# Optimization experiments

Hardware: AMD Instinct MI355X
Metric: run time of the kernel (lower is better)

## Reference

```python
import jax, jax.numpy as jnp
import numpy as np

N = 100_000        # nodes
F_IN = 1024        # input features
H1, C1 = 8, 8      # layer-1 heads, per-head channels (concat -> 64)
C_OUT = 40         # num classes (layer-2, heads=1, concat=False)
E = 3_200_000      # directed edges (avg degree 32)
NEG_SLOPE = 0.2    # PyG GATConv default leaky_relu slope


def setup_inputs() -> dict:
    key = jax.random.key(0)
    ks = jax.random.split(key, 10)
    x = jax.random.normal(ks[0], (N, F_IN), jnp.float32)
    edge_index = jax.random.randint(ks[1], (2, E), 0, N, dtype=jnp.int32)
    s1 = 1.0 / np.sqrt(F_IN)
    W1 = jax.random.normal(ks[2], (F_IN, H1 * C1), jnp.float32) * s1
    sa = 1.0 / np.sqrt(C1)
    att_src1 = jax.random.normal(ks[3], (H1, C1), jnp.float32) * sa
    att_dst1 = jax.random.normal(ks[4], (H1, C1), jnp.float32) * sa
    b1 = jnp.zeros((H1 * C1,), jnp.float32)
    s2 = 1.0 / np.sqrt(H1 * C1)
    W2 = jax.random.normal(ks[5], (H1 * C1, C_OUT), jnp.float32) * s2
    so = 1.0 / np.sqrt(C_OUT)
    att_src2 = jax.random.normal(ks[6], (1, C_OUT), jnp.float32) * so
    att_dst2 = jax.random.normal(ks[7], (1, C_OUT), jnp.float32) * so
    b2 = jnp.zeros((C_OUT,), jnp.float32)
    return {"x": x, "edge_index": edge_index, "W1": W1, "att_src1": att_src1,
            "att_dst1": att_dst1, "b1": b1, "W2": W2, "att_src2": att_src2,
            "att_dst2": att_dst2, "b2": b2}


def gat_layer(x, src, dst, W, a_src, a_dst, b, heads, ch, concat, n):
    # per-head linear projection: [n, heads, ch]
    xw = (x @ W).reshape(n, heads, ch)
    # per-node attention logits: [n, heads]
    al_src = jnp.einsum('nhc,hc->nh', xw, a_src)
    al_dst = jnp.einsum('nhc,hc->nh', xw, a_dst)
    # per-edge scores (message src -> dst): [e, heads]
    e = jax.nn.leaky_relu(al_src[src] + al_dst[dst], NEG_SLOPE)
    # segment softmax over incoming edges of each dst node
    m = jax.ops.segment_max(e, dst, num_segments=n)          # [n, heads]
    p = jnp.exp(e - m[dst])
    denom = jax.ops.segment_sum(p, dst, num_segments=n)      # [n, heads]
    alpha = p / (denom[dst] + 1e-16)                          # [e, heads]
    # weighted scatter-sum of source features
    out = jax.ops.segment_sum(xw[src] * alpha[:, :, None], dst, num_segments=n)
    out = out.reshape(n, heads * ch) if concat else out.mean(axis=1)
    return out + b


def reference(x, edge_index, W1, att_src1, att_dst1, b1, W2, att_src2, att_dst2, b2):
    n = x.shape[0]
    # PyG GATConv default: add self loops
    loop = jnp.arange(n, dtype=edge_index.dtype)
    src = jnp.concatenate([edge_index[0], loop])
    dst = jnp.concatenate([edge_index[1], loop])
    h = jax.nn.elu(gat_layer(x, src, dst, W1, att_src1, att_dst1, b1, H1, C1, True, n))
    h = gat_layer(h, src, dst, W2, att_src2, att_dst2, b2, 1, C_OUT, False, n)
    return jax.nn.log_softmax(h, axis=1)
```

## Files before the change

kernel.cpp:

```cpp
#include <hip/hip_runtime.h>
#include <hip/hip_bf16.h>
#include <cstdint>
#include <cstddef>

#define F_IN 1024
#define F1 64
#define H1 8
#define C1 8
#define C_OUT 40
#define XW2S 64
#define NEG 0.2f
#define LOG2E 1.442695040888963387f
#define B1 256
#define BSHIFT 9
#define BNODES 512

typedef __attribute__((ext_vector_type(8))) short short8;
typedef __attribute__((ext_vector_type(4))) float f32x4;

static __device__ __forceinline__ unsigned short f2bf(float f) {
  union { float f; unsigned u; } v; v.f = f;
  unsigned r = v.u + 0x7fff + ((v.u >> 16) & 1);
  return (unsigned short)(r >> 16);
}
static __device__ __forceinline__ float bf2f(unsigned short h) {
  union { unsigned u; float f; } v; v.u = ((unsigned)h) << 16; return v.f;
}
static __device__ __forceinline__ unsigned pkbf(float a, float b) {
  union { __hip_bfloat162 h; unsigned u; } c;
  c.h = __float22bfloat162_rn(float2{a, b});
  return c.u;
}
static __device__ __forceinline__ int rfl(int v) {
  return __builtin_amdgcn_readfirstlane(v);
}

__global__ __launch_bounds__(256) void w1cvt_kernel(const float* __restrict__ W1,
                                                    unsigned short* __restrict__ w1t) {
  int i = blockIdx.x * 256 + threadIdx.x;
  int c = i >> 10, k = i & 1023;
  w1t[i] = f2bf(W1[(size_t)k * F1 + c]);
}

__global__ __launch_bounds__(256) void gemm1_mfma(const float* __restrict__ x,
                                                  const unsigned short* __restrict__ w1t,
                                                  unsigned short* __restrict__ xw1, int n) {
  const int tid = threadIdx.x;
  const int wv = tid >> 6;
  const int l = tid & 63;
  const int lr = l & 15;
  const int lg = l >> 4;
  const int rowBase = blockIdx.x * 128 + wv * 32;
  int r0 = rowBase + lr, r1 = rowBase + 16 + lr;
  int r0c = r0 < n ? r0 : (n - 1);
  int r1c = r1 < n ? r1 : (n - 1);
  const float* px0 = x + (size_t)r0c * F_IN + lg * 8;
  const float* px1 = x + (size_t)r1c * F_IN + lg * 8;

  f32x4 acc00 = {0.f,0.f,0.f,0.f}, acc01 = acc00, acc02 = acc00, acc03 = acc00;
  f32x4 acc10 = acc00, acc11 = acc00, acc12 = acc00, acc13 = acc00;

#pragma unroll 2
  for (int k0 = 0; k0 < F_IN; k0 += 32) {
    float4 xa0 = *(const float4*)(px0 + k0);
    float4 xb0 = *(const float4*)(px0 + k0 + 4);
    float4 xa1 = *(const float4*)(px1 + k0);
    float4 xb1 = *(const float4*)(px1 + k0 + 4);
    union { short8 s; unsigned u[4]; } a0, a1;
    a0.u[0] = pkbf(xa0.x, xa0.y); a0.u[1] = pkbf(xa0.z, xa0.w);
    a0.u[2] = pkbf(xb0.x, xb0.y); a0.u[3] = pkbf(xb0.z, xb0.w);
    a1.u[0] = pkbf(xa1.x, xa1.y); a1.u[1] = pkbf(xa1.z, xa1.w);
    a1.u[2] = pkbf(xb1.x, xb1.y); a1.u[3] = pkbf(xb1.z, xb1.w);
    const size_t kOff = (size_t)(k0 + lg * 8);
    short8 b0 = *(const short8*)(w1t + (size_t)(0 * 16 + lr) * F_IN + kOff);
    short8 b1 = *(const short8*)(w1t + (size_t)(1 * 16 + lr) * F_IN + kOff);
    short8 b2 = *(const short8*)(w1t + (size_t)(2 * 16 + lr) * F_IN + kOff);
    short8 b3 = *(const short8*)(w1t + (size_t)(3 * 16 + lr) * F_IN + kOff);
    acc00 = __builtin_amdgcn_mfma_f32_16x16x32_bf16(a0.s, b0, acc00, 0, 0, 0);
    acc01 = __builtin_amdgcn_mfma_f32_16x16x32_bf16(a0.s, b1, acc01, 0, 0, 0);
    acc02 = __builtin_amdgcn_mfma_f32_16x16x32_bf16(a0.s, b2, acc02, 0, 0, 0);
    acc03 = __builtin_amdgcn_mfma_f32_16x16x32_bf16(a0.s, b3, acc03, 0, 0, 0);
    acc10 = __builtin_amdgcn_mfma_f32_16x16x32_bf16(a1.s, b0, acc10, 0, 0, 0);
    acc11 = __builtin_amdgcn_mfma_f32_16x16x32_bf16(a1.s, b1, acc11, 0, 0, 0);
    acc12 = __builtin_amdgcn_mfma_f32_16x16x32_bf16(a1.s, b2, acc12, 0, 0, 0);
    acc13 = __builtin_amdgcn_mfma_f32_16x16x32_bf16(a1.s, b3, acc13, 0, 0, 0);
  }

#pragma unroll
  for (int r = 0; r < 4; ++r) {
    int o0 = rowBase + lg * 4 + r;
    if (o0 < n) {
      unsigned short* po = xw1 + (size_t)o0 * F1 + lr;
      po[0]  = f2bf(acc00[r]);
      po[16] = f2bf(acc01[r]);
      po[32] = f2bf(acc02[r]);
      po[48] = f2bf(acc03[r]);
    }
    int o1 = rowBase + 16 + lg * 4 + r;
    if (o1 < n) {
      unsigned short* po = xw1 + (size_t)o1 * F1 + lr;
      po[0]  = f2bf(acc10[r]);
      po[16] = f2bf(acc11[r]);
      po[32] = f2bf(acc12[r]);
      po[48] = f2bf(acc13[r]);
    }
  }
}

__global__ __launch_bounds__(256) void al1_kernel(const unsigned short* __restrict__ xw1,
    const float* __restrict__ asrc, const float* __restrict__ adst,
    float* __restrict__ al_src, float* __restrict__ al_dst, int n) {
  int id = blockIdx.x * 256 + threadIdx.x;
  if (id >= n * H1) return;
  int node = id >> 3, h = id & 7;
  const unsigned short* row = xw1 + (size_t)node * F1 + h * C1;
  float s = 0.f, d = 0.f;
#pragma unroll
  for (int c = 0; c < C1; ++c) {
    float v = bf2f(row[c]);
    s += v * asrc[h * C1 + c];
    d += v * adst[h * C1 + c];
  }
  al_src[id] = s * LOG2E;
  al_dst[id] = d * LOG2E;
}

__global__ __launch_bounds__(256) void binhist_kernel(const int* __restrict__ dst,
    int* __restrict__ cnt, int e, int nbuck) {
  __shared__ int lh[256];
  int tid = threadIdx.x, blk = blockIdx.x;
  lh[tid] = 0;
  __syncthreads();
  int chunk = (e + gridDim.x - 1) / gridDim.x;
  int s = blk * chunk, en = min(e, s + chunk);
  for (int i = s + tid; i < en; i += 256) atomicAdd(&lh[dst[i] >> BSHIFT], 1);
  __syncthreads();
  if (tid < nbuck) cnt[tid * B1 + blk] = lh[tid];
}

__global__ __launch_bounds__(256) void scan1_kernel(const int* __restrict__ in,
    int* __restrict__ excl, int* __restrict__ bsum, int len) {
  __shared__ int s[256];
  int tid = threadIdx.x;
  int gid = blockIdx.x * 256 + tid;
  int v = gid < len ? in[gid] : 0;
  s[tid] = v;
  __syncthreads();
  for (int ofs = 1; ofs < 256; ofs <<= 1) {
    int t = (tid >= ofs) ? s[tid - ofs] : 0;
    __syncthreads();
    s[tid] += t;
    __syncthreads();
  }
  if (gid < len) excl[gid] = s[tid] - v;
  if (tid == 255) bsum[blockIdx.x] = s[255];
}

__global__ __launch_bounds__(1024) void scan2_kernel(int* __restrict__ bsum, int nb) {
  __shared__ int s[1024];
  int tid = threadIdx.x;
  int v = tid < nb ? bsum[tid] : 0;
  s[tid] = v;
  __syncthreads();
  for (int ofs = 1; ofs < 1024; ofs <<= 1) {
    int t = (tid >= ofs) ? s[tid - ofs] : 0;
    __syncthreads();
    s[tid] += t;
    __syncthreads();
  }
  if (tid < nb) bsum[tid] = s[tid] - v;
}

__global__ __launch_bounds__(256) void binscatter_kernel(const int* __restrict__ src,
    const int* __restrict__ dst, const int* __restrict__ cntS,
    const int* __restrict__ bsum, unsigned* __restrict__ binned, int e, int nbuck) {
  __shared__ int lcur[256];
  int tid = threadIdx.x, blk = blockIdx.x;
  if (tid < nbuck) lcur[tid] = cntS[tid * B1 + blk] + bsum[tid];
  __syncthreads();
  int chunk = (e + gridDim.x - 1) / gridDim.x;
  int s = blk * chunk, en = min(e, s + chunk);
  for (int i = s + tid; i < en; i += 256) {
    int d = dst[i];
    int pos = atomicAdd(&lcur[d >> BSHIFT], 1);
    binned[pos] = ((unsigned)(d & (BNODES - 1)) << 23) | (unsigned)src[i];
  }
}

__global__ __launch_bounds__(256) void bucket_csr_kernel(const unsigned* __restrict__ binned,
    const int* __restrict__ bsum, int* __restrict__ deg, int* __restrict__ off,
    int* __restrict__ csr, int e, int n, int nbuck) {
  int q = blockIdx.x, tid = threadIdx.x;
  int eBase = bsum[q];
  int eEnd = (q + 1 < nbuck) ? bsum[q + 1] : e;
  __shared__ int nh[BNODES], sc[BNODES], cu[BNODES];
  nh[tid] = 0; nh[tid + 256] = 0;
  __syncthreads();
  for (int i = eBase + tid; i < eEnd; i += 256) atomicAdd(&nh[binned[i] >> 23], 1);
  __syncthreads();
  sc[tid] = nh[tid]; sc[tid + 256] = nh[tid + 256];
  __syncthreads();
  for (int ofs = 1; ofs < BNODES; ofs <<= 1) {
    int a0 = sc[tid], a1 = sc[tid + 256];
    int b0 = (tid >= ofs) ? sc[tid - ofs] : 0;
    int b1 = (tid + 256 >= ofs) ? sc[tid + 256 - ofs] : 0;
    __syncthreads();
    sc[tid] = a0 + b0; sc[tid + 256] = a1 + b1;
    __syncthreads();
  }
  int e0 = sc[tid] - nh[tid], e1 = sc[tid + 256] - nh[tid + 256];
  cu[tid] = e0; cu[tid + 256] = e1;
  int node0 = q * BNODES + tid, node1 = node0 + 256;
  if (node0 < n) { deg[node0] = nh[tid];       off[node0] = eBase + e0; }
  if (node1 < n) { deg[node1] = nh[tid + 256]; off[node1] = eBase + e1; }
  __syncthreads();
  for (int i = eBase + tid; i < eEnd; i += 256) {
    unsigned v = binned[i];
    int pos = eBase + atomicAdd(&cu[v >> 23], 1);
    csr[pos] = (int)(v & 0x7FFFFF);
  }
}

__global__ __launch_bounds__(256) void gat1_agg(const unsigned short* __restrict__ xw1,
    const float* __restrict__ al_src, const float* __restrict__ al_dst,
    const int* __restrict__ csr, const int* __restrict__ off, const int* __restrict__ deg,
    const float* __restrict__ b1, float* __restrict__ h1, int n) {
  const int node = rfl((int)((blockIdx.x * blockDim.x + threadIdx.x) >> 6));
  if (node >= n) return;
  const int lane = threadIdx.x & 63;
  const int half = lane >> 5;
  const int c2 = lane & 31;
  const int h = c2 >> 2;
  const int base = rfl(off[node]);
  const int cnt = rfl(deg[node]);
  const float adst = al_dst[node * H1 + h];
  const int* __restrict__ csrp = csr + base;
  const char* xwB = (const char*)xw1;
  const char* alB = (const char*)al_src;
  const int cOff = c2 << 2;
  const int hOff = h << 2;

  float acc0 = 0.f, acc1 = 0.f, l = 0.f;

#define PAIR_BODY(wv_, av_) { \
    float t = (av_) + adst; \
    float sc = fmaxf(t, NEG * t); \
    float p = __builtin_amdgcn_exp2f(sc); \
    acc0 = fmaf(p, bf2f((unsigned short)((wv_) & 0xffffu)), acc0); \
    acc1 = fmaf(p, bf2f((unsigned short)((wv_) >> 16)), acc1); \
    l += p; }

  int it = 0;
  for (; it + 8 <= cnt; it += 8) {
    int xo[4];
#pragma unroll
    for (int jp = 0; jp < 4; ++jp) {
      int s0 = rfl(csrp[it + 2 * jp]) << 7;
      int s1 = rfl(csrp[it + 2 * jp + 1]) << 7;
      xo[jp] = half ? s1 : s0;
    }
    unsigned wv[4]; float av[4];
#pragma unroll
    for (int jp = 0; jp < 4; ++jp) {
      wv[jp] = *(const unsigned*)(xwB + xo[jp] + cOff);
      av[jp] = *(const float*)(alB + (xo[jp] >> 2) + hOff);
    }
#pragma unroll
    for (int jp = 0; jp < 4; ++jp) PAIR_BODY(wv[jp], av[jp]);
  }
  for (; it + 2 <= cnt; it += 2) {
    int s0 = rfl(csrp[it]) << 7;
    int s1 = rfl(csrp[it + 1]) << 7;
    int bs = half ? s1 : s0;
    unsigned w = *(const unsigned*)(xwB + bs + cOff);
    float av = *(const float*)(alB + (bs >> 2) + hOff);
    PAIR_BODY(w, av);
  }
  {
    const bool odd = (it < cnt);
    int sA = odd ? rfl(csrp[it]) : node;
    int bs = (half ? node : sA) << 7;
    unsigned w = *(const unsigned*)(xwB + bs + cOff);
    float av = *(const float*)(alB + (bs >> 2) + hOff);
    float t = av + adst;
    float sc = fmaxf(t, NEG * t);
    float p = __builtin_amdgcn_exp2f(sc);
    if (!odd && half) p = 0.f;
    acc0 = fmaf(p, bf2f((unsigned short)(w & 0xffffu)), acc0);
    acc1 = fmaf(p, bf2f((unsigned short)(w >> 16)), acc1);
    l += p;
  }
#undef PAIR_BODY

  acc0 += __shfl_xor(acc0, 32);
  acc1 += __shfl_xor(acc1, 32);
  l    += __shfl_xor(l, 32);
  if (half == 0) {
    float inv = 1.f / (l + 1e-16f);
    float2 bv = *(const float2*)(b1 + (c2 << 1));
    float o0 = acc0 * inv + bv.x;
    float o1 = acc1 * inv + bv.y;
    o0 = o0 > 0.f ? o0 : __expf(o0) - 1.f;
    o1 = o1 > 0.f ? o1 : __expf(o1) - 1.f;
    *(float2*)(h1 + (size_t)node * F1 + (c2 << 1)) = make_float2(o0, o1);
  }
}

__global__ __launch_bounds__(256) void gemm2_kernel(const float* __restrict__ h1,
    const float* __restrict__ W2, const float* __restrict__ asrc,
    const float* __restrict__ adst, unsigned short* __restrict__ xw2,
    float* __restrict__ alS2, float* __restrict__ alD2, int n) {
  __shared__ float ws[F1 * C_OUT];
  __shared__ float wsa[C_OUT], wsd[C_OUT];
  int tid = threadIdx.x;
  for (int i = tid; i < F1 * C_OUT; i += 256) ws[i] = W2[i];
  if (tid < C_OUT) { wsa[tid] = asrc[tid]; wsd[tid] = adst[tid]; }
  __syncthreads();
  int node = blockIdx.x * 256 + tid;
  if (node >= n) return;
  const float4* row4 = (const float4*)(h1 + (size_t)node * F1);
  float acc[C_OUT];
#pragma unroll
  for (int j = 0; j < C_OUT; ++j) acc[j] = 0.f;
#pragma unroll 2
  for (int k4 = 0; k4 < 16; ++k4) {
    float4 xv = row4[k4];
    const float* w0 = &ws[(4 * k4 + 0) * C_OUT];
    const float* w1 = &ws[(4 * k4 + 1) * C_OUT];
    const float* w2 = &ws[(4 * k4 + 2) * C_OUT];
    const float* w3 = &ws[(4 * k4 + 3) * C_OUT];
#pragma unroll
    for (int j = 0; j < C_OUT; j += 4) {
      float4 v0 = *(const float4*)(w0 + j);
      float4 v1 = *(const float4*)(w1 + j);
      float4 v2 = *(const float4*)(w2 + j);
      float4 v3 = *(const float4*)(w3 + j);
      acc[j + 0] += xv.x * v0.x + xv.y * v1.x + xv.z * v2.x + xv.w * v3.x;
      acc[j + 1] += xv.x * v0.y + xv.y * v1.y + xv.z * v2.y + xv.w * v3.y;
      acc[j + 2] += xv.x * v0.z + xv.y * v1.z + xv.z * v2.z + xv.w * v3.z;
      acc[j + 3] += xv.x * v0.w + xv.y * v1.w + xv.z * v2.w + xv.w * v3.w;
    }
  }
  float s = 0.f, d = 0.f;
#pragma unroll
  for (int j = 0; j < C_OUT; ++j) { s += acc[j] * wsa[j]; d += acc[j] * wsd[j]; }
  alS2[node] = s * LOG2E;
  alD2[node] = d * LOG2E;
  unsigned short* orow = xw2 + (size_t)node * XW2S;
#pragma unroll
  for (int j = 0; j < C_OUT; j += 4) {
    ushort4 o;
    o.x = f2bf(acc[j + 0]); o.y = f2bf(acc[j + 1]);
    o.z = f2bf(acc[j + 2]); o.w = f2bf(acc[j + 3]);
    *(ushort4*)(orow + j) = o;
  }
}

__global__ __launch_bounds__(256) void gat2_agg(const unsigned short* __restrict__ xw2,
    const float* __restrict__ alS, const float* __restrict__ alD,
    const int* __restrict__ csr, const int* __restrict__ off, const int* __restrict__ deg,
    const float* __restrict__ b2, float* __restrict__ out, int n) {
  const int node = rfl((int)((blockIdx.x * blockDim.x + threadIdx.x) >> 6));
  if (node >= n) return;
  const int lane = threadIdx.x & 63;
  const int half = lane >> 5;
  const int c2 = lane & 31;
  const bool act = c2 < 20;
  const int c2r = act ? c2 : 0;
  const int base = rfl(off[node]);
  const int cnt = rfl(deg[node]);
  const float adst = alD[node];
  const int* __restrict__ csrp = csr + base;
  const char* xwB = (const char*)xw2;
  const char* alB = (const char*)alS;
  const int cOff = c2r << 2;

  float acc0 = 0.f, acc1 = 0.f, l = 0.f;

#define PAIR_BODY2(wv_, av_) { \
    float t = (av_) + adst; \
    float sc = fmaxf(t, NEG * t); \
    float p = __builtin_amdgcn_exp2f(sc); \
    acc0 = fmaf(p, bf2f((unsigned short)((wv_) & 0xffffu)), acc0); \
    acc1 = fmaf(p, bf2f((unsigned short)((wv_) >> 16)), acc1); \
    l += p; }

  int it = 0;
  for (; it + 8 <= cnt; it += 8) {
    int xo[4];
#pragma unroll
    for (int jp = 0; jp < 4; ++jp) {
      int s0 = rfl(csrp[it + 2 * jp]) << 7;
      int s1 = rfl(csrp[it + 2 * jp + 1]) << 7;
      xo[jp] = half ? s1 : s0;
    }
    unsigned wv[4]; float av[4];
#pragma unroll
    for (int jp = 0; jp < 4; ++jp) {
      wv[jp] = *(const unsigned*)(xwB + xo[jp] + cOff);
      av[jp] = *(const float*)(alB + (xo[jp] >> 5));
    }
#pragma unroll
    for (int jp = 0; jp < 4; ++jp) PAIR_BODY2(wv[jp], av[jp]);
  }
  for (; it + 2 <= cnt; it += 2) {
    int s0 = rfl(csrp[it]) << 7;
    int s1 = rfl(csrp[it + 1]) << 7;
    int bs = half ? s1 : s0;
    unsigned w = *(const unsigned*)(xwB + bs + cOff);
    float av = *(const float*)(alB + (bs >> 5));
    PAIR_BODY2(w, av);
  }
  {
    const bool odd = (it < cnt);
    int sA = odd ? rfl(csrp[it]) : node;
    int bs = (half ? node : sA) << 7;
    unsigned w = *(const unsigned*)(xwB + bs + cOff);
    float av = *(const float*)(alB + (bs >> 5));
    float t = av + adst;
    float sc = fmaxf(t, NEG * t);
    float p = __builtin_amdgcn_exp2f(sc);
    if (!odd && half) p = 0.f;
    acc0 = fmaf(p, bf2f((unsigned short)(w & 0xffffu)), acc0);
    acc1 = fmaf(p, bf2f((unsigned short)(w >> 16)), acc1);
    l += p;
  }
#undef PAIR_BODY2

  acc0 += __shfl_xor(acc0, 32);
  acc1 += __shfl_xor(acc1, 32);
  l    += __shfl_xor(l, 32);

  float inv = 1.f / (l + 1e-16f);
  float v0 = -1e30f, v1 = -1e30f;
  if (act) {
    float2 bv = *(const float2*)(b2 + (c2 << 1));
    v0 = acc0 * inv + bv.x;
    v1 = acc1 * inv + bv.y;
  }
  float mx = fmaxf(v0, v1);
#pragma unroll
  for (int mask = 1; mask <= 16; mask <<= 1) mx = fmaxf(mx, __shfl_xor(mx, mask));
  float e0 = act ? __expf(v0 - mx) : 0.f;
  float e1 = act ? __expf(v1 - mx) : 0.f;
  float sum = e0 + e1;
#pragma unroll
  for (int mask = 1; mask <= 16; mask <<= 1) sum += __shfl_xor(sum, mask);
  if (half == 0 && act) {
    float ls = __logf(sum);
    *(float2*)(out + (size_t)node * C_OUT + (c2 << 1)) =
        make_float2(v0 - mx - ls, v1 - mx - ls);
  }
}

extern "C" void kernel_launch(void* const* d_in, const int* in_sizes, int n_in,
                              void* d_out, int out_size, void* d_ws, size_t ws_size,
                              hipStream_t stream) {
  const float* x   = (const float*)d_in[0];
  const int*   ei  = (const int*)d_in[1];
  const float* W1  = (const float*)d_in[2];
  const float* as1 = (const float*)d_in[3];
  const float* ad1 = (const float*)d_in[4];
  const float* b1  = (const float*)d_in[5];
  const float* W2  = (const float*)d_in[6];
  const float* as2 = (const float*)d_in[7];
  const float* ad2 = (const float*)d_in[8];
  const float* b2  = (const float*)d_in[9];
  float* out = (float*)d_out;

  const int n = in_sizes[0] / F_IN;
  const int e = in_sizes[1] / 2;
  const int* srcIdx = ei;
  const int* dstIdx = ei + e;
  const int nbuck = (n + BNODES - 1) >> BSHIFT;
  const int clen = nbuck * B1;

  char* p = (char*)d_ws;
  auto take = [&](size_t bytes) {
    char* q = p;
    p += (bytes + 255) & ~(size_t)255;
    return q;
  };
  unsigned short* xw1 = (unsigned short*)take((size_t)n * F1 * 2);
  float* h1           = (float*)take((size_t)n * F1 * 4);
  unsigned short* xw2 = (unsigned short*)take((size_t)n * XW2S * 2);
  unsigned short* w1t = (unsigned short*)take((size_t)F_IN * F1 * 2);
  float* alS1 = (float*)take((size_t)n * H1 * 4);
  float* alD1 = (float*)take((size_t)n * H1 * 4);
  float* alS2 = (float*)take((size_t)n * 4);
  float* alD2 = (float*)take((size_t)n * 4);
  int* deg  = (int*)take((size_t)n * 4);
  int* offb = (int*)take((size_t)n * 4);
  int* cnt  = (int*)take((size_t)clen * 4);
  int* cntS = (int*)take((size_t)clen * 4);
  int* bsum = (int*)take(4096);
  unsigned* binned = (unsigned*)take((size_t)e * 4);
  int* csr  = (int*)take((size_t)e * 4);

  dim3 b256(256);
  w1cvt_kernel<<<dim3((F_IN * F1) / 256), b256, 0, stream>>>(W1, w1t);
  gemm1_mfma<<<dim3((n + 127) / 128), b256, 0, stream>>>(x, w1t, xw1, n);
  al1_kernel<<<dim3((n * H1 + 255) / 256), b256, 0, stream>>>(xw1, as1, ad1, alS1, alD1, n);

  binhist_kernel<<<dim3(B1), b256, 0, stream>>>(dstIdx, cnt, e, nbuck);
  int nbScan = (clen + 255) / 256;
  scan1_kernel<<<dim3(nbScan), b256, 0, stream>>>(cnt, cntS, bsum, clen);
  scan2_kernel<<<dim3(1), dim3(1024), 0, stream>>>(bsum, nbScan);
  binscatter_kernel<<<dim3(B1), b256, 0, stream>>>(srcIdx, dstIdx, cntS, bsum, binned, e, nbuck);
  bucket_csr_kernel<<<dim3(nbuck), b256, 0, stream>>>(binned, bsum, deg, offb, csr, e, n, nbuck);

  gat1_agg<<<dim3((n + 3) / 4), b256, 0, stream>>>(xw1, alS1, alD1, csr, offb, deg, b1, h1, n);
  gemm2_kernel<<<dim3((n + 255) / 256), b256, 0, stream>>>(h1, W2, as2, ad2, xw2, alS2, alD2, n);
  gat2_agg<<<dim3((n + 3) / 4), b256, 0, stream>>>(xw2, alS2, alD2, csr, offb, deg, b2, out, n);
}
```

Measured before the change: 440.8 us.

## Fuse edge histogram into GEMM1 launch, shrink buckets, deepen aggregation unroll

Merges the destination-bucket histogram into the first GEMM kernel as extra blocks, so the histogram overlaps the GEMM and one launch is removed. Halves the bucket size to 256 nodes, so each bucket_csr block handles one node per thread and scans fewer elements, at the cost of more buckets and a longer count scan. Also vectorizes the per-node attention logit load and doubles the gather unroll in both aggregation kernels to put more loads in flight, which raises register pressure.

After: 408.7 us. 7.3% less time.

```diff
diff --git a/kernel.cpp b/kernel.cpp
--- a/kernel.cpp
+++ b/kernel.cpp
@@ -12,8 +12,8 @@
 #define NEG 0.2f
 #define LOG2E 1.442695040888963387f
 #define B1 256
-#define BSHIFT 9
-#define BNODES 512
+#define BSHIFT 8
+#define BNODES 256
 
 typedef __attribute__((ext_vector_type(8))) short short8;
 typedef __attribute__((ext_vector_type(4))) float f32x4;
@@ -42,15 +42,28 @@
   w1t[i] = f2bf(W1[(size_t)k * F1 + c]);
 }
 
-__global__ __launch_bounds__(256) void gemm1_mfma(const float* __restrict__ x,
-                                                  const unsigned short* __restrict__ w1t,
-                                                  unsigned short* __restrict__ xw1, int n) {
+__global__ __launch_bounds__(256) void k1_hist_gemm(const float* __restrict__ x,
+    const unsigned short* __restrict__ w1t, unsigned short* __restrict__ xw1,
+    const int* __restrict__ dst, int* __restrict__ cnt, int n, int e, int nbuck) {
+  const int bid = blockIdx.x;
   const int tid = threadIdx.x;
+  if (bid < B1) {
+    __shared__ int lh[512];
+    lh[tid] = 0; lh[tid + 256] = 0;
+    __syncthreads();
+    int chunk = (e + B1 - 1) / B1;
+    int s = bid * chunk, en = min(e, s + chunk);
+    for (int i = s + tid; i < en; i += 256) atomicAdd(&lh[dst[i] >> BSHIFT], 1);
+    __syncthreads();
+    for (int b = tid; b < nbuck; b += 256) cnt[b * B1 + bid] = lh[b];
+    return;
+  }
+  const int gb = bid - B1;
   const int wv = tid >> 6;
   const int l = tid & 63;
   const int lr = l & 15;
   const int lg = l >> 4;
-  const int rowBase = blockIdx.x * 128 + wv * 32;
+  const int rowBase = gb * 128 + wv * 32;
   int r0 = rowBase + lr, r1 = rowBase + 16 + lr;
   int r0c = r0 < n ? r0 : (n - 1);
   int r1c = r1 < n ? r1 : (n - 1);
@@ -113,29 +126,17 @@
   int id = blockIdx.x * 256 + threadIdx.x;
   if (id >= n * H1) return;
   int node = id >> 3, h = id & 7;
-  const unsigned short* row = xw1 + (size_t)node * F1 + h * C1;
+  union { short8 s; unsigned short u[8]; } rowv;
+  rowv.s = *(const short8*)(xw1 + (size_t)node * F1 + h * C1);
   float s = 0.f, d = 0.f;
 #pragma unroll
   for (int c = 0; c < C1; ++c) {
-    float v = bf2f(row[c]);
+    float v = bf2f(rowv.u[c]);
     s += v * asrc[h * C1 + c];
     d += v * adst[h * C1 + c];
   }
   al_src[id] = s * LOG2E;
   al_dst[id] = d * LOG2E;
-}
-
-__global__ __launch_bounds__(256) void binhist_kernel(const int* __restrict__ dst,
-    int* __restrict__ cnt, int e, int nbuck) {
-  __shared__ int lh[256];
-  int tid = threadIdx.x, blk = blockIdx.x;
-  lh[tid] = 0;
-  __syncthreads();
-  int chunk = (e + gridDim.x - 1) / gridDim.x;
-  int s = blk * chunk, en = min(e, s + chunk);
-  for (int i = s + tid; i < en; i += 256) atomicAdd(&lh[dst[i] >> BSHIFT], 1);
-  __syncthreads();
-  if (tid < nbuck) cnt[tid * B1 + blk] = lh[tid];
 }
 
 __global__ __launch_bounds__(256) void scan1_kernel(const int* __restrict__ in,
@@ -174,9 +175,9 @@
 __global__ __launch_bounds__(256) void binscatter_kernel(const int* __restrict__ src,
     const int* __restrict__ dst, const int* __restrict__ cntS,
     const int* __restrict__ bsum, unsigned* __restrict__ binned, int e, int nbuck) {
-  __shared__ int lcur[256];
+  __shared__ int lcur[512];
   int tid = threadIdx.x, blk = blockIdx.x;
-  if (tid < nbuck) lcur[tid] = cntS[tid * B1 + blk] + bsum[tid];
+  for (int b = tid; b < nbuck; b += 256) lcur[b] = cntS[b * B1 + blk] + bsum[b];
   __syncthreads();
   int chunk = (e + gridDim.x - 1) / gridDim.x;
   int s = blk * chunk, en = min(e, s + chunk);
@@ -194,30 +195,28 @@
   int eBase = bsum[q];
   int eEnd = (q + 1 < nbuck) ? bsum[q + 1] : e;
   __shared__ int nh[BNODES], sc[BNODES], cu[BNODES];
-  nh[tid] = 0; nh[tid + 256] = 0;
+  nh[tid] = 0;
   __syncthreads();
   for (int i = eBase + tid; i < eEnd; i += 256) atomicAdd(&nh[binned[i] >> 23], 1);
   __syncthreads();
-  sc[tid] = nh[tid]; sc[tid + 256] = nh[tid + 256];
+  int v = nh[tid];
+  sc[tid] = v;
   __syncthreads();
   for (int ofs = 1; ofs < BNODES; ofs <<= 1) {
-    int a0 = sc[tid], a1 = sc[tid + 256];
-    int b0 = (tid >= ofs) ? sc[tid - ofs] : 0;
-    int b1 = (tid + 256 >= ofs) ? sc[tid + 256 - ofs] : 0;
-    __syncthreads();
-    sc[tid] = a0 + b0; sc[tid + 256] = a1 + b1;
-    __syncthreads();
-  }
-  int e0 = sc[tid] - nh[tid], e1 = sc[tid + 256] - nh[tid + 256];
-  cu[tid] = e0; cu[tid + 256] = e1;
-  int node0 = q * BNODES + tid, node1 = node0 + 256;
-  if (node0 < n) { deg[node0] = nh[tid];       off[node0] = eBase + e0; }
-  if (node1 < n) { deg[node1] = nh[tid + 256]; off[node1] = eBase + e1; }
+    int t = (tid >= ofs) ? sc[tid - ofs] : 0;
+    __syncthreads();
+    sc[tid] += t;
+    __syncthreads();
+  }
+  int ex = sc[tid] - v;
+  cu[tid] = ex;
+  int node0 = q * BNODES + tid;
+  if (node0 < n) { deg[node0] = v; off[node0] = eBase + ex; }
   __syncthreads();
   for (int i = eBase + tid; i < eEnd; i += 256) {
-    unsigned v = binned[i];
-    int pos = eBase + atomicAdd(&cu[v >> 23], 1);
-    csr[pos] = (int)(v & 0x7FFFFF);
+    unsigned w = binned[i];
+    int pos = eBase + atomicAdd(&cu[w >> 23], 1);
+    csr[pos] = (int)(w & 0x7FFFFF);
   }
 }
 
@@ -251,22 +250,22 @@
     l += p; }
 
   int it = 0;
-  for (; it + 8 <= cnt; it += 8) {
-    int xo[4];
-#pragma unroll
-    for (int jp = 0; jp < 4; ++jp) {
+  for (; it + 16 <= cnt; it += 16) {
+    int xo[8];
+#pragma unroll
+    for (int jp = 0; jp < 8; ++jp) {
       int s0 = rfl(csrp[it + 2 * jp]) << 7;
       int s1 = rfl(csrp[it + 2 * jp + 1]) << 7;
       xo[jp] = half ? s1 : s0;
     }
-    unsigned wv[4]; float av[4];
-#pragma unroll
-    for (int jp = 0; jp < 4; ++jp) {
+    unsigned wv[8]; float av[8];
+#pragma unroll
+    for (int jp = 0; jp < 8; ++jp) {
       wv[jp] = *(const unsigned*)(xwB + xo[jp] + cOff);
       av[jp] = *(const float*)(alB + (xo[jp] >> 2) + hOff);
     }
 #pragma unroll
-    for (int jp = 0; jp < 4; ++jp) PAIR_BODY(wv[jp], av[jp]);
+    for (int jp = 0; jp < 8; ++jp) PAIR_BODY(wv[jp], av[jp]);
   }
   for (; it + 2 <= cnt; it += 2) {
     int s0 = rfl(csrp[it]) << 7;
@@ -386,22 +385,22 @@
     l += p; }
 
   int it = 0;
-  for (; it + 8 <= cnt; it += 8) {
-    int xo[4];
-#pragma unroll
-    for (int jp = 0; jp < 4; ++jp) {
+  for (; it + 16 <= cnt; it += 16) {
+    int xo[8];
+#pragma unroll
+    for (int jp = 0; jp < 8; ++jp) {
       int s0 = rfl(csrp[it + 2 * jp]) << 7;
       int s1 = rfl(csrp[it + 2 * jp + 1]) << 7;
       xo[jp] = half ? s1 : s0;
     }
-    unsigned wv[4]; float av[4];
-#pragma unroll
-    for (int jp = 0; jp < 4; ++jp) {
+    unsigned wv[8]; float av[8];
+#pragma unroll
+    for (int jp = 0; jp < 8; ++jp) {
       wv[jp] = *(const unsigned*)(xwB + xo[jp] + cOff);
       av[jp] = *(const float*)(alB + (xo[jp] >> 5));
     }
 #pragma unroll
-    for (int jp = 0; jp < 4; ++jp) PAIR_BODY2(wv[jp], av[jp]);
+    for (int jp = 0; jp < 8; ++jp) PAIR_BODY2(wv[jp], av[jp]);
   }
   for (; it + 2 <= cnt; it += 2) {
     int s0 = rfl(csrp[it]) << 7;
@@ -498,11 +497,11 @@
   int* csr  = (int*)take((size_t)e * 4);
 
   dim3 b256(256);
+  const int gB = (n + 127) / 128;
   w1cvt_kernel<<<dim3((F_IN * F1) / 256), b256, 0, stream>>>(W1, w1t);
-  gemm1_mfma<<<dim3((n + 127) / 128), b256, 0, stream>>>(x, w1t, xw1, n);
+  k1_hist_gemm<<<dim3(B1 + gB), b256, 0, stream>>>(x, w1t, xw1, dstIdx, cnt, n, e, nbuck);
   al1_kernel<<<dim3((n * H1 + 255) / 256), b256, 0, stream>>>(xw1, as1, ad1, alS1, alD1, n);
 
-  binhist_kernel<<<dim3(B1), b256, 0, stream>>>(dstIdx, cnt, e, nbuck);
   int nbScan = (clen + 255) / 256;
   scan1_kernel<<<dim3(nbScan), b256, 0, stream>>>(cnt, cntS, bsum, clen);
   scan2_kernel<<<dim3(1), dim3(1024), 0, stream>>>(bsum, nbScan);
```
